# Performance work log

Measured on AMD Instinct MI355X. Metric: run time of the kernel, lower is better.

The kernel has to match this reference:

```python
import jax, jax.numpy as jnp
import numpy as np

DIM = 512
HEADS = 8
DHEAD = 64
SCALE = DHEAD ** -0.5
EPS = 1e-5


def ln(x, g, b):
    mu = jnp.mean(x, axis=-1, keepdims=True)
    var = jnp.var(x, axis=-1, keepdims=True)
    return (x - mu) * jax.lax.rsqrt(var + EPS) * g + b


def heads(t):
    b, n, _ = t.shape
    return t.reshape(b, n, HEADS, DHEAD).transpose(0, 2, 1, 3)  # b h n d


def unheads(t):
    b, h, n, d = t.shape
    return t.transpose(0, 2, 1, 3).reshape(b, n, h * d)


def attn(q, k, v):
    dots = jnp.einsum('bhid,bhjd->bhij', q, k) * SCALE
    a = jax.nn.softmax(dots, axis=-1)
    return unheads(jnp.einsum('bhij,bhjd->bhid', a, v))


def setup_inputs() -> dict:
    key = jax.random.key(0)
    ks = jax.random.split(key, 12)
    s = 0.02
    inp = {
        'x': jax.random.normal(ks[0], (4, 2048, DIM), jnp.float32),
        'y': jax.random.normal(ks[1], (4, 1024, DIM), jnp.float32),
        'sa_g': jnp.ones((DIM,), jnp.float32),
        'sa_b': jnp.zeros((DIM,), jnp.float32),
        'sa_wqkv': jax.random.normal(ks[2], (DIM, 3 * HEADS * DHEAD), jnp.float32) * s,
        'sa_wo': jax.random.normal(ks[3], (HEADS * DHEAD, DIM), jnp.float32) * s,
        'sa_bo': jnp.zeros((DIM,), jnp.float32),
        'n1_g': jnp.ones((DIM,), jnp.float32),
        'n1_b': jnp.zeros((DIM,), jnp.float32),
        'ca_g': jnp.ones((DIM,), jnp.float32),
        'ca_b': jnp.zeros((DIM,), jnp.float32),
        'ca_wq': jax.random.normal(ks[4], (DIM, HEADS * DHEAD), jnp.float32) * s,
        'ca_wkv': jax.random.normal(ks[5], (DIM, 2 * HEADS * DHEAD), jnp.float32) * s,
        'ca_wo': jax.random.normal(ks[6], (HEADS * DHEAD, DIM), jnp.float32) * s,
        'ca_bo': jnp.zeros((DIM,), jnp.float32),
        'ff_g': jnp.ones((DIM,), jnp.float32),
        'ff_b': jnp.zeros((DIM,), jnp.float32),
        'ff_w1': jax.random.normal(ks[7], (DIM, 4 * DIM), jnp.float32) * s,
        'ff_b1': jnp.zeros((4 * DIM,), jnp.float32),
        'ff_w2': jax.random.normal(ks[8], (4 * DIM, DIM), jnp.float32) * s,
        'ff_b2': jnp.zeros((DIM,), jnp.float32),
        'shot_num': 1,
    }
    return inp


def reference(x, y, sa_g, sa_b, sa_wqkv, sa_wo, sa_bo, n1_g, n1_b,
              ca_g, ca_b, ca_wq, ca_wkv, ca_wo, ca_bo,
              ff_g, ff_b, ff_w1, ff_b1, ff_w2, ff_b2, shot_num):
    # --- self-attention (has its own pre-LN) ---
    xn = ln(x, sa_g, sa_b)
    qkv = xn @ sa_wqkv
    q, k, v = (heads(t) for t in jnp.split(qkv, 3, axis=-1))
    x = x + attn(q, k, v) @ sa_wo + sa_bo
    # --- cross-attention: norm1 outside, CrossAttentionB norms x again; y un-normed ---
    xn = ln(ln(x, n1_g, n1_b), ca_g, ca_b)
    q = heads(xn @ ca_wq)
    kv = y @ ca_wkv
    k, v = (heads(t) for t in jnp.split(kv, 2, axis=-1))
    x = x + attn(q, k, v) @ ca_wo + ca_bo
    # --- MLP with pre-LN, exact GELU ---
    xn = ln(x, ff_g, ff_b)
    h = jax.nn.gelu(xn @ ff_w1 + ff_b1, approximate=False)
    x = x + h @ ff_w2 + ff_b2
    return x
```

## Files before the change

### kernel.cpp

```cpp
#include <hip/hip_runtime.h>
#include <hip/hip_bf16.h>
#include <math.h>

#define DIM    512
#define HEADS  8
#define DHEAD  64
#define BATCH  4
#define NQ     2048
#define NKV    1024
#define ATT_SCALE 0.125f
#define LN_EPS 1e-5f

typedef unsigned short u16;
typedef float f32x4 __attribute__((ext_vector_type(4)));
typedef short bf16x8 __attribute__((ext_vector_type(8)));

__device__ __forceinline__ u16 f2bf(float f) {
    unsigned u = __float_as_uint(f);
    u += 0x7fffu + ((u >> 16) & 1u);
    return (u16)(u >> 16);
}

__device__ __forceinline__ float gelu_f(float x) {
    return 0.5f * x * (1.0f + erff(x * 0.70710678118654752440f));
}

__global__ __launch_bounds__(256)
void f2b_kernel(const float* __restrict__ in, u16* __restrict__ out, int n4)
{
    int i = blockIdx.x * 256 + threadIdx.x;
    if (i < n4) {
        float4 v = *(const float4*)&in[(size_t)i * 4];
        unsigned lo = f2bf(v.x) | ((unsigned)f2bf(v.y) << 16);
        unsigned hi = f2bf(v.z) | ((unsigned)f2bf(v.w) << 16);
        *(uint2*)&out[(size_t)i * 4] = make_uint2(lo, hi);
    }
}

__global__ __launch_bounds__(256)
void wtrans_kernel(const float* __restrict__ src, u16* __restrict__ dst,
                   int K, int N)
{
    __shared__ float tile[32][33];
    const int n0 = blockIdx.x * 32, k0 = blockIdx.y * 32;
    const int tx = threadIdx.x & 31, ty = threadIdx.x >> 5;
#pragma unroll
    for (int j = 0; j < 4; ++j)
        tile[ty + 8 * j][tx] = src[(size_t)(k0 + ty + 8 * j) * N + n0 + tx];
    __syncthreads();
#pragma unroll
    for (int j = 0; j < 4; ++j)
        dst[(size_t)(n0 + ty + 8 * j) * K + k0 + tx] = f2bf(tile[tx][ty + 8 * j]);
}

__global__ __launch_bounds__(128)
void ln_kernel(const float* __restrict__ x, const float* __restrict__ g,
               const float* __restrict__ b, u16* __restrict__ out)
{
    __shared__ float red[4];
    const int row = blockIdx.x;
    const int t = threadIdx.x;
    const int wid = t >> 6, lane = t & 63;

    float4 v = *(const float4*)&x[(size_t)row * DIM + t * 4];
    float s  = v.x + v.y + v.z + v.w;
    float sq = v.x*v.x + v.y*v.y + v.z*v.z + v.w*v.w;
#pragma unroll
    for (int off = 32; off >= 1; off >>= 1) {
        s  += __shfl_xor(s, off);
        sq += __shfl_xor(sq, off);
    }
    if (lane == 0) { red[wid] = s; red[2 + wid] = sq; }
    __syncthreads();
    s = red[0] + red[1]; sq = red[2] + red[3];

    const float mu = s * (1.0f / DIM);
    const float rs = rsqrtf(sq * (1.0f / DIM) - mu * mu + LN_EPS);
    float4 gv = *(const float4*)&g[t * 4];
    float4 bv = *(const float4*)&b[t * 4];
    float ox = (v.x - mu) * rs * gv.x + bv.x;
    float oy = (v.y - mu) * rs * gv.y + bv.y;
    float oz = (v.z - mu) * rs * gv.z + bv.z;
    float ow = (v.w - mu) * rs * gv.w + bv.w;
    unsigned lo = f2bf(ox) | ((unsigned)f2bf(oy) << 16);
    unsigned hi = f2bf(oz) | ((unsigned)f2bf(ow) << 16);
    *(uint2*)&out[(size_t)row * DIM + t * 4] = make_uint2(lo, hi);
}

__global__ __launch_bounds__(128)
void ln2_kernel(const float* __restrict__ x,
                const float* __restrict__ g1, const float* __restrict__ b1,
                const float* __restrict__ g2, const float* __restrict__ b2,
                u16* __restrict__ out)
{
    __shared__ float red[4];
    const int row = blockIdx.x;
    const int t = threadIdx.x;
    const int wid = t >> 6, lane = t & 63;

    float4 v = *(const float4*)&x[(size_t)row * DIM + t * 4];
    float s  = v.x + v.y + v.z + v.w;
    float sq = v.x*v.x + v.y*v.y + v.z*v.z + v.w*v.w;
#pragma unroll
    for (int off = 32; off >= 1; off >>= 1) {
        s  += __shfl_xor(s, off);
        sq += __shfl_xor(sq, off);
    }
    if (lane == 0) { red[wid] = s; red[2 + wid] = sq; }
    __syncthreads();
    s = red[0] + red[1]; sq = red[2] + red[3];
    float mu = s * (1.0f / DIM);
    float rs = rsqrtf(sq * (1.0f / DIM) - mu * mu + LN_EPS);

    float4 g = *(const float4*)&g1[t * 4];
    float4 bb = *(const float4*)&b1[t * 4];
    float4 z;
    z.x = (v.x - mu) * rs * g.x + bb.x;
    z.y = (v.y - mu) * rs * g.y + bb.y;
    z.z = (v.z - mu) * rs * g.z + bb.z;
    z.w = (v.w - mu) * rs * g.w + bb.w;

    s  = z.x + z.y + z.z + z.w;
    sq = z.x*z.x + z.y*z.y + z.z*z.z + z.w*z.w;
#pragma unroll
    for (int off = 32; off >= 1; off >>= 1) {
        s  += __shfl_xor(s, off);
        sq += __shfl_xor(sq, off);
    }
    __syncthreads();
    if (lane == 0) { red[wid] = s; red[2 + wid] = sq; }
    __syncthreads();
    s = red[0] + red[1]; sq = red[2] + red[3];
    mu = s * (1.0f / DIM);
    rs = rsqrtf(sq * (1.0f / DIM) - mu * mu + LN_EPS);

    g  = *(const float4*)&g2[t * 4];
    bb = *(const float4*)&b2[t * 4];
    float ox = (z.x - mu) * rs * g.x + bb.x;
    float oy = (z.y - mu) * rs * g.y + bb.y;
    float oz = (z.z - mu) * rs * g.z + bb.z;
    float ow = (z.w - mu) * rs * g.w + bb.w;
    unsigned lo = f2bf(ox) | ((unsigned)f2bf(oy) << 16);
    unsigned hi = f2bf(oz) | ((unsigned)f2bf(ow) << 16);
    *(uint2*)&out[(size_t)row * DIM + t * 4] = make_uint2(lo, hi);
}

template<int EPI>
__global__ __launch_bounds__(256)
void gemm_bf16(const u16* __restrict__ A, const u16* __restrict__ BT,
               const float* __restrict__ bias, const float* __restrict__ res,
               void* __restrict__ Cv, int M, int K, int Nc)
{
    __shared__ __align__(16) u16 As[128][40];
    __shared__ __align__(16) u16 Bs[128][40];

    const int t    = threadIdx.x;
    const int lane = t & 63;
    const int w    = t >> 6;
    const int wr   = (w >> 1) * 64, wc = (w & 1) * 64;
    const int rlo  = lane & 15, rhi = lane >> 4;
    const int row0 = blockIdx.y * 128, col0 = blockIdx.x * 128;

    const f32x4 z4 = {0.f, 0.f, 0.f, 0.f};
    f32x4 acc[4][4];
#pragma unroll
    for (int m = 0; m < 4; ++m)
#pragma unroll
        for (int n = 0; n < 4; ++n) acc[m][n] = z4;

    uint4 pa[2], pb[2];
    const int nkt = K >> 5;

#define LOADG(kt)                                                            \
    {                                                                        \
        _Pragma("unroll")                                                    \
        for (int i = 0; i < 2; ++i) {                                        \
            int idx = i * 256 + t, r = idx >> 2, c = idx & 3;                \
            pa[i] = *(const uint4*)&A[(size_t)(row0 + r) * K + (kt)*32 + c*8];\
            pb[i] = *(const uint4*)&BT[(size_t)(col0 + r) * K + (kt)*32 + c*8];\
        }                                                                    \
    }

    LOADG(0);
    for (int kt = 0; kt < nkt; ++kt) {
        __syncthreads();
#pragma unroll
        for (int i = 0; i < 2; ++i) {
            int idx = i * 256 + t, r = idx >> 2, c = idx & 3;
            *(uint4*)&As[r][c * 8] = pa[i];
            *(uint4*)&Bs[r][c * 8] = pb[i];
        }
        __syncthreads();
        if (kt + 1 < nkt) LOADG(kt + 1);

        bf16x8 af[4], bf[4];
#pragma unroll
        for (int m = 0; m < 4; ++m)
            af[m] = *(const bf16x8*)&As[wr + m * 16 + rlo][rhi * 8];
#pragma unroll
        for (int n = 0; n < 4; ++n)
            bf[n] = *(const bf16x8*)&Bs[wc + n * 16 + rlo][rhi * 8];
#pragma unroll
        for (int m = 0; m < 4; ++m)
#pragma unroll
            for (int n = 0; n < 4; ++n)
                acc[m][n] = __builtin_amdgcn_mfma_f32_16x16x32_bf16(
                    af[m], bf[n], acc[m][n], 0, 0, 0);
    }
#undef LOADG

    float* Cf = (float*)Cv;
    u16*   Cb = (u16*)Cv;
#pragma unroll
    for (int m = 0; m < 4; ++m) {
#pragma unroll
        for (int n = 0; n < 4; ++n) {
            const int cg = col0 + wc + n * 16 + rlo;
            const float bv = (EPI >= 2) ? bias[cg] : 0.0f;
#pragma unroll
            for (int i = 0; i < 4; ++i) {
                const size_t rg = (size_t)(row0 + wr + m * 16 + rhi * 4 + i);
                float val = acc[m][n][i] + bv;
                if (EPI == 3) val = gelu_f(val);
                if (EPI == 2) {
                    val += res[rg * Nc + cg];
                    Cf[rg * Nc + cg] = val;
                } else {
                    Cb[rg * Nc + cg] = f2bf(val);
                }
            }
        }
    }
}

__global__ __launch_bounds__(256)
void attn_mfma(const u16* __restrict__ Q, int qs,
               const u16* __restrict__ K, const u16* __restrict__ V, int kvs,
               u16* __restrict__ O, int n_q, int n_k)
{
    __shared__ __align__(16) u16 Qs[64][72];
    __shared__ __align__(16) u16 Ks[64][72];
    __shared__ __align__(16) u16 VT[64][72];
    __shared__ __align__(16) u16 Ps[64][72];

    const int t    = threadIdx.x;
    const int lane = t & 63;
    const int w    = t >> 6;
    const int wq   = w * 16;
    const int rlo  = lane & 15, rhi = lane >> 4;
    const int bh = blockIdx.y, b = bh >> 3, h = bh & 7;
    const int q0 = blockIdx.x * 64;

    const u16* Qb = Q + (size_t)b * n_q * qs + h * DHEAD;
    const u16* Kb = K + (size_t)b * n_k * kvs + h * DHEAD;
    const u16* Vb = V + (size_t)b * n_k * kvs + h * DHEAD;

#pragma unroll
    for (int i = 0; i < 2; ++i) {
        int idx = i * 256 + t, r = idx >> 3, c = idx & 7;
        *(uint4*)&Qs[r][c * 8] = *(const uint4*)&Qb[(size_t)(q0 + r) * qs + c * 8];
    }

    const f32x4 z4 = {0.f, 0.f, 0.f, 0.f};
    f32x4 o_acc[4] = {z4, z4, z4, z4};
    float m_i[4] = {-1e30f, -1e30f, -1e30f, -1e30f};
    float l_i[4] = {0.f, 0.f, 0.f, 0.f};

    const int ntiles = n_k >> 6;
    for (int it = 0; it < ntiles; ++it) {
        __syncthreads();
#pragma unroll
        for (int i = 0; i < 2; ++i) {
            int idx = i * 256 + t, r = idx >> 3, c = idx & 7;
            *(uint4*)&Ks[r][c * 8] =
                *(const uint4*)&Kb[(size_t)(it * 64 + r) * kvs + c * 8];
            uint4 vv = *(const uint4*)&Vb[(size_t)(it * 64 + r) * kvs + c * 8];
            u16 e[8];
            *(uint4*)e = vv;
            const int kvw = r ^ ((c & 7) << 3);
#pragma unroll
            for (int q = 0; q < 8; ++q)
                VT[c * 8 + q][kvw] = e[q];
        }
        __syncthreads();

        bf16x8 aq[2];
#pragma unroll
        for (int kb = 0; kb < 2; ++kb)
            aq[kb] = *(const bf16x8*)&Qs[wq + rlo][kb * 32 + rhi * 8];
        f32x4 s[4] = {z4, z4, z4, z4};
#pragma unroll
        for (int n = 0; n < 4; ++n)
#pragma unroll
            for (int kb = 0; kb < 2; ++kb) {
                bf16x8 bk = *(const bf16x8*)&Ks[n * 16 + rlo][kb * 32 + rhi * 8];
                s[n] = __builtin_amdgcn_mfma_f32_16x16x32_bf16(aq[kb], bk, s[n], 0, 0, 0);
            }
#pragma unroll
        for (int n = 0; n < 4; ++n) s[n] *= ATT_SCALE;

#pragma unroll
        for (int i = 0; i < 4; ++i) {
            float mx = fmaxf(fmaxf(s[0][i], s[1][i]), fmaxf(s[2][i], s[3][i]));
#pragma unroll
            for (int off = 1; off < 16; off <<= 1) mx = fmaxf(mx, __shfl_xor(mx, off));
            float mnew  = fmaxf(m_i[i], mx);
            float alpha = __expf(m_i[i] - mnew);
            float rsum = 0.f;
#pragma unroll
            for (int n = 0; n < 4; ++n) {
                float p = __expf(s[n][i] - mnew);
                rsum += p;
                Ps[wq + rhi * 4 + i][n * 16 + rlo] = f2bf(p);
            }
#pragma unroll
            for (int off = 1; off < 16; off <<= 1) rsum += __shfl_xor(rsum, off);
            l_i[i] = l_i[i] * alpha + rsum;
            m_i[i] = mnew;
#pragma unroll
            for (int n = 0; n < 4; ++n) o_acc[n][i] *= alpha;
        }

#pragma unroll
        for (int kb = 0; kb < 2; ++kb) {
            bf16x8 pa = *(const bf16x8*)&Ps[wq + rlo][kb * 32 + rhi * 8];
#pragma unroll
            for (int n = 0; n < 4; ++n) {
                const int d = n * 16 + rlo;
                const int kvb2 = (kb * 32 + rhi * 8) ^ (((d >> 3) & 7) << 3);
                bf16x8 bv = *(const bf16x8*)&VT[d][kvb2];
                o_acc[n] = __builtin_amdgcn_mfma_f32_16x16x32_bf16(pa, bv, o_acc[n], 0, 0, 0);
            }
        }
    }

#pragma unroll
    for (int i = 0; i < 4; ++i) {
        const float inv = 1.0f / l_i[i];
        const size_t orow = ((size_t)b * n_q + q0 + wq + rhi * 4 + i) * DIM + h * DHEAD;
#pragma unroll
        for (int n = 0; n < 4; ++n)
            O[orow + n * 16 + rlo] = f2bf(o_acc[n][i] * inv);
    }
}

extern "C" void kernel_launch(void* const* d_in, const int* in_sizes, int n_in,
                              void* d_out, int out_size, void* d_ws, size_t ws_size,
                              hipStream_t stream)
{
    const float* x       = (const float*)d_in[0];
    const float* y       = (const float*)d_in[1];
    const float* sa_g    = (const float*)d_in[2];
    const float* sa_b    = (const float*)d_in[3];
    const float* sa_wqkv = (const float*)d_in[4];
    const float* sa_wo   = (const float*)d_in[5];
    const float* sa_bo   = (const float*)d_in[6];
    const float* n1_g    = (const float*)d_in[7];
    const float* n1_b    = (const float*)d_in[8];
    const float* ca_g    = (const float*)d_in[9];
    const float* ca_b    = (const float*)d_in[10];
    const float* ca_wq   = (const float*)d_in[11];
    const float* ca_wkv  = (const float*)d_in[12];
    const float* ca_wo   = (const float*)d_in[13];
    const float* ca_bo   = (const float*)d_in[14];
    const float* ff_g    = (const float*)d_in[15];
    const float* ff_b    = (const float*)d_in[16];
    const float* ff_w1   = (const float*)d_in[17];
    const float* ff_b1   = (const float*)d_in[18];
    const float* ff_w2   = (const float*)d_in[19];
    const float* ff_b2   = (const float*)d_in[20];
    float* out = (float*)d_out;

    const int Mx = BATCH * NQ;
    const int My = BATCH * NKV;

    u16* xb    = (u16*)d_ws;
    u16* bigb  = xb    + 4194304;
    u16* attb  = bigb  + 16777216;
    u16* q2b   = attb  + 4194304;
    u16* kvb   = q2b   + 4194304;
    u16* ybb   = kvb   + 4194304;
    u16* wqkvT = ybb   + 2097152;
    u16* woT   = wqkvT + 786432;
    u16* caqT  = woT   + 262144;
    u16* cakvT = caqT  + 262144;
    u16* caoT  = cakvT + 524288;
    u16* w1T   = caoT  + 262144;
    u16* w2T   = w1T   + 1048576;

    f2b_kernel<<<(My * DIM / 4 + 255) / 256, 256, 0, stream>>>(y, ybb, My * DIM / 4);
    wtrans_kernel<<<dim3(1536 / 32, 512 / 32),  256, 0, stream>>>(sa_wqkv, wqkvT, 512, 1536);
    wtrans_kernel<<<dim3(512 / 32,  512 / 32),  256, 0, stream>>>(sa_wo,   woT,   512, 512);
    wtrans_kernel<<<dim3(512 / 32,  512 / 32),  256, 0, stream>>>(ca_wq,   caqT,  512, 512);
    wtrans_kernel<<<dim3(1024 / 32, 512 / 32),  256, 0, stream>>>(ca_wkv,  cakvT, 512, 1024);
    wtrans_kernel<<<dim3(512 / 32,  512 / 32),  256, 0, stream>>>(ca_wo,   caoT,  512, 512);
    wtrans_kernel<<<dim3(2048 / 32, 512 / 32),  256, 0, stream>>>(ff_w1,   w1T,   512, 2048);
    wtrans_kernel<<<dim3(512 / 32,  2048 / 32), 256, 0, stream>>>(ff_w2,   w2T,   2048, 512);

    ln_kernel<<<Mx, 128, 0, stream>>>(x, sa_g, sa_b, xb);
    gemm_bf16<0><<<dim3(1536 / 128, Mx / 128), 256, 0, stream>>>(
        xb, wqkvT, nullptr, nullptr, bigb, Mx, 512, 1536);
    attn_mfma<<<dim3(NQ / 64, BATCH * HEADS), 256, 0, stream>>>(
        bigb, 1536, bigb + 512, bigb + 1024, 1536, attb, NQ, NQ);
    gemm_bf16<2><<<dim3(512 / 128, Mx / 128), 256, 0, stream>>>(
        attb, woT, sa_bo, x, out, Mx, 512, 512);

    ln2_kernel<<<Mx, 128, 0, stream>>>(out, n1_g, n1_b, ca_g, ca_b, xb);
    gemm_bf16<0><<<dim3(512 / 128, Mx / 128), 256, 0, stream>>>(
        xb, caqT, nullptr, nullptr, q2b, Mx, 512, 512);
    gemm_bf16<0><<<dim3(1024 / 128, My / 128), 256, 0, stream>>>(
        ybb, cakvT, nullptr, nullptr, kvb, My, 512, 1024);
    attn_mfma<<<dim3(NQ / 64, BATCH * HEADS), 256, 0, stream>>>(
        q2b, 512, kvb, kvb + 512, 1024, attb, NQ, NKV);
    gemm_bf16<2><<<dim3(512 / 128, Mx / 128), 256, 0, stream>>>(
        attb, caoT, ca_bo, out, out, Mx, 512, 512);

    ln_kernel<<<Mx, 128, 0, stream>>>(out, ff_g, ff_b, xb);
    gemm_bf16<3><<<dim3(2048 / 128, Mx / 128), 256, 0, stream>>>(
        xb, w1T, ff_b1, nullptr, bigb, Mx, 512, 2048);
    gemm_bf16<2><<<dim3(512 / 128, Mx / 128), 256, 0, stream>>>(
        bigb, w2T, ff_b2, out, out, Mx, 2048, 512);

    (void)in_sizes; (void)n_in; (void)out_size; (void)ws_size;
}
```

Measured before the change: 694.2 us.

## Rewrite flash attention with 32x32 MFMA, register-resident P and lazy rescaling

Replaces the 16x16 MFMA attention kernel with one that computes transposed scores (K·Q^T) using 32x32x16 MFMAs, so each wave owns 32 query rows and the block covers 128 queries. Softmax probabilities stay in registers and are repacked with permlane32_swap instead of going through shared memory. The kernel also uses exp2 with the scale folded into Q and skips the running-max rescale unless the max grows by more than a threshold. The intent is to cut LDS traffic, shuffle reductions and exp work. It halves the grid, which lowers occupancy, and relies on gfx950-specific instructions.

```diff
diff --git a/kernel.cpp b/kernel.cpp
--- a/kernel.cpp
+++ b/kernel.cpp
@@ -12,13 +12,20 @@
 #define LN_EPS 1e-5f
 
 typedef unsigned short u16;
-typedef float f32x4 __attribute__((ext_vector_type(4)));
+typedef float f32x4  __attribute__((ext_vector_type(4)));
+typedef float f32x16 __attribute__((ext_vector_type(16)));
 typedef short bf16x8 __attribute__((ext_vector_type(8)));
 
 __device__ __forceinline__ u16 f2bf(float f) {
     unsigned u = __float_as_uint(f);
     u += 0x7fffu + ((u >> 16) & 1u);
     return (u16)(u >> 16);
+}
+
+__device__ __forceinline__ unsigned cvtpk_bf16(float lo, float hi) {
+    unsigned r;
+    asm("v_cvt_pk_bf16_f32 %0, %1, %2" : "=v"(r) : "v"(lo), "v"(hi));
+    return r;
 }
 
 __device__ __forceinline__ float gelu_f(float x) {
@@ -234,37 +241,48 @@
 }
 
 __global__ __launch_bounds__(256)
-void attn_mfma(const u16* __restrict__ Q, int qs,
-               const u16* __restrict__ K, const u16* __restrict__ V, int kvs,
-               u16* __restrict__ O, int n_q, int n_k)
-{
-    __shared__ __align__(16) u16 Qs[64][72];
+void attn_mfma2(const u16* __restrict__ Q, int qs,
+                const u16* __restrict__ K, const u16* __restrict__ V, int kvs,
+                u16* __restrict__ O, int n_q, int n_k)
+{
     __shared__ __align__(16) u16 Ks[64][72];
     __shared__ __align__(16) u16 VT[64][72];
-    __shared__ __align__(16) u16 Ps[64][72];
 
     const int t    = threadIdx.x;
     const int lane = t & 63;
     const int w    = t >> 6;
-    const int wq   = w * 16;
-    const int rlo  = lane & 15, rhi = lane >> 4;
+    const int ql   = lane & 31;
+    const int hi   = lane >> 5;
     const int bh = blockIdx.y, b = bh >> 3, h = bh & 7;
-    const int q0 = blockIdx.x * 64;
+    const int q0 = blockIdx.x * 128;
 
     const u16* Qb = Q + (size_t)b * n_q * qs + h * DHEAD;
     const u16* Kb = K + (size_t)b * n_k * kvs + h * DHEAD;
     const u16* Vb = V + (size_t)b * n_k * kvs + h * DHEAD;
 
-#pragma unroll
-    for (int i = 0; i < 2; ++i) {
-        int idx = i * 256 + t, r = idx >> 3, c = idx & 7;
-        *(uint4*)&Qs[r][c * 8] = *(const uint4*)&Qb[(size_t)(q0 + r) * qs + c * 8];
-    }
-
-    const f32x4 z4 = {0.f, 0.f, 0.f, 0.f};
-    f32x4 o_acc[4] = {z4, z4, z4, z4};
-    float m_i[4] = {-1e30f, -1e30f, -1e30f, -1e30f};
-    float l_i[4] = {0.f, 0.f, 0.f, 0.f};
+    const float QSC = ATT_SCALE * 1.44269504088896f;
+    bf16x8 qf[4];
+    {
+        const u16* Qrow = Qb + (size_t)(q0 + w * 32 + ql) * qs;
+#pragma unroll
+        for (int kb = 0; kb < 4; ++kb) {
+            uint4 raw = *(const uint4*)&Qrow[kb * 16 + hi * 8];
+            u16 e[8]; *(uint4*)e = raw;
+            union { unsigned u[4]; bf16x8 v; } uq;
+#pragma unroll
+            for (int j = 0; j < 4; ++j) {
+                float lo = __uint_as_float((unsigned)e[2*j]     << 16) * QSC;
+                float hf = __uint_as_float((unsigned)e[2*j + 1] << 16) * QSC;
+                uq.u[j] = cvtpk_bf16(lo, hf);
+            }
+            qf[kb] = uq.v;
+        }
+    }
+
+    const f32x16 z16 = {0.f,0.f,0.f,0.f,0.f,0.f,0.f,0.f,
+                        0.f,0.f,0.f,0.f,0.f,0.f,0.f,0.f};
+    f32x16 oa0 = z16, oa1 = z16;
+    float m = -1e30f, l = 0.f;
 
     const int ntiles = n_k >> 6;
     for (int it = 0; it < ntiles; ++it) {
@@ -275,8 +293,7 @@
             *(uint4*)&Ks[r][c * 8] =
                 *(const uint4*)&Kb[(size_t)(it * 64 + r) * kvs + c * 8];
             uint4 vv = *(const uint4*)&Vb[(size_t)(it * 64 + r) * kvs + c * 8];
-            u16 e[8];
-            *(uint4*)e = vv;
+            u16 e[8]; *(uint4*)e = vv;
             const int kvw = r ^ ((c & 7) << 3);
 #pragma unroll
             for (int q = 0; q < 8; ++q)
@@ -284,63 +301,94 @@
         }
         __syncthreads();
 
-        bf16x8 aq[2];
-#pragma unroll
-        for (int kb = 0; kb < 2; ++kb)
-            aq[kb] = *(const bf16x8*)&Qs[wq + rlo][kb * 32 + rhi * 8];
-        f32x4 s[4] = {z4, z4, z4, z4};
-#pragma unroll
-        for (int n = 0; n < 4; ++n)
-#pragma unroll
-            for (int kb = 0; kb < 2; ++kb) {
-                bf16x8 bk = *(const bf16x8*)&Ks[n * 16 + rlo][kb * 32 + rhi * 8];
-                s[n] = __builtin_amdgcn_mfma_f32_16x16x32_bf16(aq[kb], bk, s[n], 0, 0, 0);
-            }
-#pragma unroll
-        for (int n = 0; n < 4; ++n) s[n] *= ATT_SCALE;
-
-#pragma unroll
-        for (int i = 0; i < 4; ++i) {
-            float mx = fmaxf(fmaxf(s[0][i], s[1][i]), fmaxf(s[2][i], s[3][i]));
-#pragma unroll
-            for (int off = 1; off < 16; off <<= 1) mx = fmaxf(mx, __shfl_xor(mx, off));
-            float mnew  = fmaxf(m_i[i], mx);
-            float alpha = __expf(m_i[i] - mnew);
-            float rsum = 0.f;
-#pragma unroll
-            for (int n = 0; n < 4; ++n) {
-                float p = __expf(s[n][i] - mnew);
-                rsum += p;
-                Ps[wq + rhi * 4 + i][n * 16 + rlo] = f2bf(p);
-            }
-#pragma unroll
-            for (int off = 1; off < 16; off <<= 1) rsum += __shfl_xor(rsum, off);
-            l_i[i] = l_i[i] * alpha + rsum;
-            m_i[i] = mnew;
-#pragma unroll
-            for (int n = 0; n < 4; ++n) o_acc[n][i] *= alpha;
-        }
-
-#pragma unroll
-        for (int kb = 0; kb < 2; ++kb) {
-            bf16x8 pa = *(const bf16x8*)&Ps[wq + rlo][kb * 32 + rhi * 8];
-#pragma unroll
-            for (int n = 0; n < 4; ++n) {
-                const int d = n * 16 + rlo;
-                const int kvb2 = (kb * 32 + rhi * 8) ^ (((d >> 3) & 7) << 3);
-                bf16x8 bv = *(const bf16x8*)&VT[d][kvb2];
-                o_acc[n] = __builtin_amdgcn_mfma_f32_16x16x32_bf16(pa, bv, o_acc[n], 0, 0, 0);
-            }
-        }
-    }
-
-#pragma unroll
-    for (int i = 0; i < 4; ++i) {
-        const float inv = 1.0f / l_i[i];
-        const size_t orow = ((size_t)b * n_q + q0 + wq + rhi * 4 + i) * DIM + h * DHEAD;
-#pragma unroll
-        for (int n = 0; n < 4; ++n)
-            O[orow + n * 16 + rlo] = f2bf(o_acc[n][i] * inv);
+        f32x16 s0 = z16, s1 = z16;
+#pragma unroll
+        for (int kb = 0; kb < 4; ++kb) {
+            bf16x8 a0 = *(const bf16x8*)&Ks[ql]     [kb * 16 + hi * 8];
+            bf16x8 a1 = *(const bf16x8*)&Ks[32 + ql][kb * 16 + hi * 8];
+            s0 = __builtin_amdgcn_mfma_f32_32x32x16_bf16(a0, qf[kb], s0, 0, 0, 0);
+            s1 = __builtin_amdgcn_mfma_f32_32x32x16_bf16(a1, qf[kb], s1, 0, 0, 0);
+        }
+
+        float a[16];
+#pragma unroll
+        for (int i = 0; i < 16; ++i) a[i] = fmaxf(s0[i], s1[i]);
+#pragma unroll
+        for (int i = 0; i < 8; ++i) a[i] = fmaxf(a[i], a[i + 8]);
+#pragma unroll
+        for (int i = 0; i < 4; ++i) a[i] = fmaxf(a[i], a[i + 4]);
+        a[0] = fmaxf(a[0], a[2]); a[1] = fmaxf(a[1], a[3]);
+        a[0] = fmaxf(a[0], a[1]);
+        float pmax = fmaxf(a[0], __shfl_xor(a[0], 32));
+
+        if (!__all(pmax - m <= 5.0f)) {
+            float mn = fmaxf(m, pmax);
+            float al = __builtin_amdgcn_exp2f(m - mn);
+            l *= al; oa0 *= al; oa1 *= al;
+            m = mn;
+        }
+
+        f32x16 pe0, pe1;
+        float sc[16];
+#pragma unroll
+        for (int i = 0; i < 16; ++i) {
+            pe0[i] = __builtin_amdgcn_exp2f(s0[i] - m);
+            pe1[i] = __builtin_amdgcn_exp2f(s1[i] - m);
+            sc[i]  = pe0[i] + pe1[i];
+        }
+#pragma unroll
+        for (int i = 0; i < 8; ++i) sc[i] += sc[i + 8];
+#pragma unroll
+        for (int i = 0; i < 4; ++i) sc[i] += sc[i + 4];
+        float rsum = (sc[0] + sc[1]) + (sc[2] + sc[3]);
+        rsum += __shfl_xor(rsum, 32);
+        l += rsum;
+
+#define PV_STEP(PE, KB2)                                                     \
+        {                                                                    \
+            const int w2 = ((KB2) & 1) * 8;                                  \
+            unsigned Xw = cvtpk_bf16(PE[w2 + 0], PE[w2 + 1]);                \
+            unsigned Zw = cvtpk_bf16(PE[w2 + 2], PE[w2 + 3]);                \
+            unsigned Yw = cvtpk_bf16(PE[w2 + 4], PE[w2 + 5]);                \
+            unsigned Ww = cvtpk_bf16(PE[w2 + 6], PE[w2 + 7]);                \
+            asm volatile("v_permlane32_swap_b32 %0, %1"                      \
+                         : "+v"(Yw), "+v"(Xw));                              \
+            asm volatile("v_permlane32_swap_b32 %0, %1"                      \
+                         : "+v"(Ww), "+v"(Zw));                              \
+            union { unsigned u[4]; bf16x8 v; } pa_;                          \
+            pa_.u[0] = Xw; pa_.u[1] = Zw; pa_.u[2] = Yw; pa_.u[3] = Ww;      \
+            {                                                                \
+                const int d0 = ql;                                           \
+                const int c0 = ((KB2) * 16 + hi * 8) ^ (((d0 >> 3) & 7) << 3);\
+                bf16x8 vb = *(const bf16x8*)&VT[d0][c0];                     \
+                oa0 = __builtin_amdgcn_mfma_f32_32x32x16_bf16(vb, pa_.v, oa0, 0, 0, 0); \
+            }                                                                \
+            {                                                                \
+                const int d1 = 32 + ql;                                      \
+                const int c1 = ((KB2) * 16 + hi * 8) ^ (((d1 >> 3) & 7) << 3);\
+                bf16x8 vb = *(const bf16x8*)&VT[d1][c1];                     \
+                oa1 = __builtin_amdgcn_mfma_f32_32x32x16_bf16(vb, pa_.v, oa1, 0, 0, 0); \
+            }                                                                \
+        }
+        PV_STEP(pe0, 0)
+        PV_STEP(pe0, 1)
+        PV_STEP(pe1, 2)
+        PV_STEP(pe1, 3)
+#undef PV_STEP
+    }
+
+    const float inv = 1.0f / l;
+    const size_t orow = (size_t)b * n_q + q0 + w * 32 + ql;
+    u16* Op = O + orow * DIM + h * DHEAD;
+#pragma unroll
+    for (int g = 0; g < 4; ++g) {
+        const int dbase = 8 * g + 4 * hi;
+        unsigned w0 = cvtpk_bf16(oa0[4*g + 0] * inv, oa0[4*g + 1] * inv);
+        unsigned w1 = cvtpk_bf16(oa0[4*g + 2] * inv, oa0[4*g + 3] * inv);
+        *(uint2*)&Op[dbase] = make_uint2(w0, w1);
+        unsigned w2 = cvtpk_bf16(oa1[4*g + 0] * inv, oa1[4*g + 1] * inv);
+        unsigned w3 = cvtpk_bf16(oa1[4*g + 2] * inv, oa1[4*g + 3] * inv);
+        *(uint2*)&Op[32 + dbase] = make_uint2(w2, w3);
     }
 }
 
@@ -400,7 +448,7 @@
     ln_kernel<<<Mx, 128, 0, stream>>>(x, sa_g, sa_b, xb);
     gemm_bf16<0><<<dim3(1536 / 128, Mx / 128), 256, 0, stream>>>(
         xb, wqkvT, nullptr, nullptr, bigb, Mx, 512, 1536);
-    attn_mfma<<<dim3(NQ / 64, BATCH * HEADS), 256, 0, stream>>>(
+    attn_mfma2<<<dim3(NQ / 128, BATCH * HEADS), 256, 0, stream>>>(
         bigb, 1536, bigb + 512, bigb + 1024, 1536, attb, NQ, NQ);
     gemm_bf16<2><<<dim3(512 / 128, Mx / 128), 256, 0, stream>>>(
         attb, woT, sa_bo, x, out, Mx, 512, 512);
@@ -410,7 +458,7 @@
         xb, caqT, nullptr, nullptr, q2b, Mx, 512, 512);
     gemm_bf16<0><<<dim3(1024 / 128, My / 128), 256, 0, stream>>>(
         ybb, cakvT, nullptr, nullptr, kvb, My, 512, 1024);
-    attn_mfma<<<dim3(NQ / 64, BATCH * HEADS), 256, 0, stream>>>(
+    attn_mfma2<<<dim3(NQ / 128, BATCH * HEADS), 256, 0, stream>>>(
         q2b, 512, kvb, kvb + 512, 1024, attb, NQ, NKV);
     gemm_bf16<2><<<dim3(512 / 128, Mx / 128), 256, 0, stream>>>(
         attb, caoT, ca_bo, out, out, Mx, 512, 512);
```

Measured after the change: 587.9 us. 1.18x faster.
